# Kernel optimization log

Measured on AMD Instinct MI355X. Metric: run time of the kernel, lower is better.

Reference implementation:

```python
import jax, jax.numpy as jnp
import numpy as np

B, S, D, H = 2, 2048, 1024, 16
DK = D // H  # 64
THETA = 10000.0


def setup_inputs() -> dict:
    key = jax.random.key(0)
    ks = jax.random.split(key, 5)
    scale = 1.0 / np.sqrt(D)
    return {
        "x": jax.random.normal(ks[0], (B, S, D), dtype=jnp.float32),
        "Wq": jax.random.normal(ks[1], (D, D), dtype=jnp.float32) * scale,
        "Wk": jax.random.normal(ks[2], (D, D), dtype=jnp.float32) * scale,
        "Wv": jax.random.normal(ks[3], (D, D), dtype=jnp.float32) * scale,
        "Wo": jax.random.normal(ks[4], (D, D), dtype=jnp.float32) * scale,
    }


def _rope(t):
    # t: (B, H, S, DK); interleaved-pair rotary embedding with positions 0..S-1
    s = t.shape[-2]
    inv_freq = 1.0 / (THETA ** (jnp.arange(0, DK, 2, dtype=jnp.float32) / DK))  # (DK/2,)
    ang = jnp.arange(s, dtype=jnp.float32)[:, None] * inv_freq[None, :]  # (S, DK/2)
    cos, sin = jnp.cos(ang), jnp.sin(ang)
    x1 = t[..., 0::2]
    x2 = t[..., 1::2]
    r1 = x1 * cos - x2 * sin
    r2 = x1 * sin + x2 * cos
    return jnp.stack([r1, r2], axis=-1).reshape(t.shape)


def reference(x, Wq, Wk, Wv, Wo):
    # Projections (Linear: y = x @ W^T), split heads -> (B, H, S, DK)
    def proj(W):
        y = jnp.einsum('bsd,ed->bse', x, W)
        return y.reshape(B, S, H, DK).transpose(0, 2, 1, 3)

    Q = _rope(proj(Wq))
    K = _rope(proj(Wk))
    V = proj(Wv)

    scores = jnp.einsum('bhqd,bhkd->bhqk', Q, K)
    scores = jnp.clip(scores, -80.0, 80.0)
    causal = jnp.tril(jnp.ones((S, S), dtype=bool))  # (S, S)
    scores = jnp.where(causal, scores, -jnp.inf)
    weights = jax.nn.softmax(scores / np.sqrt(DK), axis=-1)
    att = jnp.einsum('bhqk,bhkd->bhqd', weights, V)
    att = att.transpose(0, 2, 1, 3).reshape(B, S, D)
    return jnp.einsum('bsd,ed->bse', att, Wo)
```

## Files before the change

kernel.cpp:

```cpp
#include <hip/hip_runtime.h>
#include <hip/hip_bf16.h>

#define B_  2
#define S_  2048
#define D_  1024
#define H_  16
#define DK_ 64
#define BH_ (B_*H_)
#define M_  (B_*S_)

typedef __attribute__((ext_vector_type(8))) short bf16x8;
typedef __attribute__((ext_vector_type(4))) float f32x4;

__device__ inline float bf2f(unsigned short u) {
    return __uint_as_float(((unsigned)u) << 16);
}
__device__ inline unsigned short f2bf(float f) {
    unsigned u = __float_as_uint(f);
    u += 0x7fffu + ((u >> 16) & 1u);
    return (unsigned short)(u >> 16);
}
__device__ inline unsigned short f2bf_hw(float f) {
    __hip_bfloat16 h = __float2bfloat16(f);
    return *reinterpret_cast<unsigned short*>(&h);
}
__device__ inline unsigned packbf2(float lo, float hi) {
    return (unsigned)f2bf_hw(lo) | ((unsigned)f2bf_hw(hi) << 16);
}

__device__ inline void gld16(const void* g, void* l) {
    __builtin_amdgcn_global_load_lds(
        (const __attribute__((address_space(1))) unsigned int*)g,
        (__attribute__((address_space(3))) unsigned int*)l, 16, 0, 0);
}

__global__ void cast_f32_to_bf16(const float* __restrict__ src,
                                 unsigned short* __restrict__ dst, int n) {
    int i = (blockIdx.x * blockDim.x + threadIdx.x) * 4;
    int stride = gridDim.x * blockDim.x * 4;
    for (int j = i; j < n; j += stride) {
        float4 v = *reinterpret_cast<const float4*>(src + j);
        ushort4 o;
        o.x = f2bf(v.x); o.y = f2bf(v.y); o.z = f2bf(v.z); o.w = f2bf(v.w);
        *reinterpret_cast<ushort4*>(dst + j) = o;
    }
}

__global__ void cast4_f32_to_bf16(const float* __restrict__ s0, const float* __restrict__ s1,
                                  const float* __restrict__ s2, const float* __restrict__ s3,
                                  unsigned short* __restrict__ d0, unsigned short* __restrict__ d1,
                                  unsigned short* __restrict__ d2, unsigned short* __restrict__ d3) {
    const float* s; unsigned short* d;
    switch (blockIdx.y) {
        case 0: s = s0; d = d0; break;
        case 1: s = s1; d = d1; break;
        case 2: s = s2; d = d2; break;
        default: s = s3; d = d3; break;
    }
    int j = (blockIdx.x * blockDim.x + threadIdx.x) * 4;
    float4 v = *reinterpret_cast<const float4*>(s + j);
    ushort4 o;
    o.x = f2bf(v.x); o.y = f2bf(v.y); o.z = f2bf(v.z); o.w = f2bf(v.w);
    *reinterpret_cast<ushort4*>(d + j) = o;
}

#define BMQ 128
#define BNQ 128

__global__ __launch_bounds__(256)
void gemm_qkv(const unsigned short* __restrict__ A, const unsigned short* __restrict__ Wcat,
              unsigned short* __restrict__ Qf, unsigned short* __restrict__ Kf,
              unsigned short* __restrict__ Vf) {
    __shared__ unsigned short As[BMQ * 64];
    __shared__ unsigned short Bs[BNQ * 64];
    const int K = D_;
    const int tid  = threadIdx.x;
    const int lane = tid & 63;
    const int wid  = tid >> 6;
    const int wm = wid & 1, wn = wid >> 1;
    const int m0 = blockIdx.y * BMQ, n0 = blockIdx.x * BNQ;
    const int g  = lane >> 4, cl = lane & 15;

    f32x4 acc[4][4];
#pragma unroll
    for (int i = 0; i < 4; i++)
#pragma unroll
        for (int j = 0; j < 4; j++) acc[i][j] = f32x4{0.f, 0.f, 0.f, 0.f};

    const int srow = tid >> 3;
    const unsigned short* Asrc[4];
    const unsigned short* Bsrc[4];
#pragma unroll
    for (int q = 0; q < 4; q++) {
        int row = srow + q * 32;
        Asrc[q] = A    + (long)(m0 + row) * K + (((tid & 7) ^ (srow & 7)) * 8);
        Bsrc[q] = Wcat + (long)(n0 + row) * K + (((tid & 7) ^ (srow & 7)) * 8);
    }

    for (int k0 = 0; k0 < K; k0 += 64) {
        __syncthreads();
#pragma unroll
        for (int q = 0; q < 4; q++) gld16(Asrc[q] + k0, As + tid * 8 + q * 2048);
#pragma unroll
        for (int q = 0; q < 4; q++) gld16(Bsrc[q] + k0, Bs + tid * 8 + q * 2048);
        __syncthreads();

#pragma unroll
        for (int kk = 0; kk < 2; kk++) {
            bf16x8 af[4], bfr[4];
#pragma unroll
            for (int i = 0; i < 4; i++) {
                int row = wm*64 + i*16 + cl;
                af[i]  = *reinterpret_cast<const bf16x8*>(As + row * 64 + (((kk*4 + g) ^ (cl & 7)) * 8));
            }
#pragma unroll
            for (int j = 0; j < 4; j++) {
                int row = wn*64 + j*16 + cl;
                bfr[j] = *reinterpret_cast<const bf16x8*>(Bs + row * 64 + (((kk*4 + g) ^ (cl & 7)) * 8));
            }
#pragma unroll
            for (int i = 0; i < 4; i++)
#pragma unroll
                for (int j = 0; j < 4; j++)
                    acc[i][j] = __builtin_amdgcn_mfma_f32_16x16x32_bf16(af[i], bfr[j], acc[i][j], 0, 0, 0);
        }
    }

    const int mat = n0 >> 10;
    if (mat < 2) {
        float invf[4];
#pragma unroll
        for (int jj = 0; jj < 4; jj++)
            invf[jj] = exp2f(-(float)(jj*8 + (cl >> 1)) * 0.4152410118569779f);
#pragma unroll
        for (int i = 0; i < 4; i++) {
#pragma unroll
            for (int jj = 0; jj < 4; jj++) {
                const int gcl = (n0 & 1023) + wn*64 + jj*16 + cl;
                const int hh = gcl >> 6;
                const int dk = jj*16 + cl;
#pragma unroll
                for (int rr = 0; rr < 4; rr++) {
                    int gr = m0 + wm*64 + i*16 + g*4 + rr;
                    int bb = gr >> 11, s = gr & (S_ - 1);
                    float v = acc[i][jj][rr];
                    float p = __shfl_xor(v, 1);
                    float ang = (float)s * invf[jj];
                    float sn = __sinf(ang), cs = __cosf(ang);
                    float r = (cl & 1) ? fmaf(v, cs, p * sn) : fmaf(v, cs, -p * sn);
                    long idx;
                    if (mat == 0) {
                        const int lane_p = (s & 15) | (((dk >> 3) & 3) << 4);
                        idx = ((long)(bb*H_ + hh) * 128 + (s >> 4)) * 1024
                            + (dk >> 5) * 512 + lane_p * 8 + (dk & 7);
                        Qf[idx] = f2bf_hw(r);
                    } else {
                        const int vv = s & 63;
                        const int ng = ((vv >> 5) << 1) | ((vv >> 2) & 1);
                        const int slot = ((vv & 31) >> 3) * 4 + (vv & 3);
                        const int lane_p = slot | (((dk >> 3) & 3) << 4);
                        idx = (((long)(bb*H_ + hh) * 32 + (s >> 6)) * 4 + ng) * 1024
                            + (dk >> 5) * 512 + lane_p * 8 + (dk & 7);
                        Kf[idx] = f2bf_hw(r);
                    }
                }
            }
        }
    } else {
#pragma unroll
        for (int i = 0; i < 4; i++) {
#pragma unroll
            for (int jj = 0; jj < 4; jj++) {
                const int gcl = (n0 & 1023) + wn*64 + jj*16 + cl;
                const int hh = gcl >> 6;
                const int sbase = m0 + wm*64 + i*16 + g*4;
                const int bb = sbase >> 11, s0l = sbase & (S_ - 1);
                const int lane_p = cl | (((s0l >> 3) & 3) << 4);
                const int e0 = s0l & 7;
                ushort4 o;
                o.x = f2bf_hw(acc[i][jj][0]); o.y = f2bf_hw(acc[i][jj][1]);
                o.z = f2bf_hw(acc[i][jj][2]); o.w = f2bf_hw(acc[i][jj][3]);
                long idx = ((long)(bb*H_ + hh) * 4 + jj) * 32768
                         + (long)(s0l >> 5) * 512 + lane_p * 8 + e0;
                *reinterpret_cast<ushort4*>(Vf + idx) = o;
            }
        }
    }
}

#define BM 64
#define BN 128

__global__ __launch_bounds__(256)
void gemm_out(const unsigned short* __restrict__ A, const unsigned short* __restrict__ Bw,
              float* __restrict__ Cf) {
    __shared__ unsigned short As[BM * 64];
    __shared__ unsigned short Bs[BN * 64];
    const int K = D_;
    const int tid  = threadIdx.x;
    const int lane = tid & 63;
    const int wid  = tid >> 6;
    const int wm = wid & 1, wn = wid >> 1;
    const int m0 = blockIdx.y * BM, n0 = blockIdx.x * BN;
    const int g  = lane >> 4, cl = lane & 15;

    f32x4 acc[2][4];
#pragma unroll
    for (int i = 0; i < 2; i++)
#pragma unroll
        for (int j = 0; j < 4; j++) acc[i][j] = f32x4{0.f, 0.f, 0.f, 0.f};

    const int srow = tid >> 3;
    const unsigned short* Asrc[2];
    const unsigned short* Bsrc[4];
#pragma unroll
    for (int q = 0; q < 2; q++) {
        int row = srow + q * 32;
        Asrc[q] = A + (long)(m0 + row) * K + (((tid & 7) ^ (srow & 7)) * 8);
    }
#pragma unroll
    for (int q = 0; q < 4; q++) {
        int row = srow + q * 32;
        Bsrc[q] = Bw + (long)(n0 + row) * K + (((tid & 7) ^ (srow & 7)) * 8);
    }

    for (int k0 = 0; k0 < K; k0 += 64) {
        __syncthreads();
#pragma unroll
        for (int q = 0; q < 2; q++) gld16(Asrc[q] + k0, As + tid * 8 + q * 2048);
#pragma unroll
        for (int q = 0; q < 4; q++) gld16(Bsrc[q] + k0, Bs + tid * 8 + q * 2048);
        __syncthreads();

#pragma unroll
        for (int kk = 0; kk < 2; kk++) {
            bf16x8 af[2], bfr[4];
#pragma unroll
            for (int i = 0; i < 2; i++) {
                int row = wm*32 + i*16 + cl;
                af[i]  = *reinterpret_cast<const bf16x8*>(As + row * 64 + (((kk*4 + g) ^ (cl & 7)) * 8));
            }
#pragma unroll
            for (int j = 0; j < 4; j++) {
                int row = wn*64 + j*16 + cl;
                bfr[j] = *reinterpret_cast<const bf16x8*>(Bs + row * 64 + (((kk*4 + g) ^ (cl & 7)) * 8));
            }
#pragma unroll
            for (int i = 0; i < 2; i++)
#pragma unroll
                for (int j = 0; j < 4; j++)
                    acc[i][j] = __builtin_amdgcn_mfma_f32_16x16x32_bf16(af[i], bfr[j], acc[i][j], 0, 0, 0);
        }
    }

#pragma unroll
    for (int i = 0; i < 2; i++)
#pragma unroll
        for (int j = 0; j < 4; j++)
#pragma unroll
            for (int rr = 0; rr < 4; rr++) {
                int gr = m0 + wm*32 + i*16 + g*4 + rr;
                int gc = n0 + wn*64 + j*16 + cl;
                Cf[(long)gr * D_ + gc] = acc[i][j][rr];
            }
}

#define WQ    32
#define KVBLK 64

__global__ __launch_bounds__(256)
void flash_attn(const unsigned short* __restrict__ Qf, const unsigned short* __restrict__ Kf,
                const unsigned short* __restrict__ Vf, unsigned short* __restrict__ Att) {
    __shared__ __align__(16) char smem[17408];
    const int tid  = threadIdx.x;
    const int lane = tid & 63;
    const int wid  = tid >> 6;
    const int g = lane >> 4, cl = lane & 15;
    const int bh = blockIdx.x & (BH_ - 1);
    const int pr = blockIdx.x >> 5;
    const int b = bh >> 4, h = bh & (H_ - 1);

    f32x4* Ol = reinterpret_cast<f32x4*>(smem);
    float* Ll = reinterpret_cast<float*>(smem + 16384);

    const unsigned short* Qb = Qf + (long)bh * 131072;
    const unsigned short* Kb = Kf + (long)bh * 131072;
    const unsigned short* Vb = Vf + (long)bh * 131072;

    const float RS = 0.125f * 1.44269504f;
    const float RB = -10.f * 1.44269504f;

    for (int half = 0; half < 2; half++) {
        const int qt = half ? (S_/WQ - 1 - pr) : pr;
        const int q0 = qt * WQ;
        const int nt = (q0 + WQ + KVBLK - 1) / KVBLK;

        bf16x8 aq[2][2];
#pragma unroll
        for (int m = 0; m < 2; m++)
#pragma unroll
            for (int c = 0; c < 2; c++)
                aq[m][c] = *reinterpret_cast<const bf16x8*>(Qb + ((q0 >> 4) + m) * 1024 + c * 512 + lane * 8);

        f32x4 o[2][4];
#pragma unroll
        for (int m = 0; m < 2; m++)
#pragma unroll
            for (int t = 0; t < 4; t++) o[m][t] = f32x4{0.f, 0.f, 0.f, 0.f};
        float lp[2] = {0.f, 0.f};

        for (int j = wid; j < nt; j += 4) {
            const int kv0 = j * KVBLK;
            bf16x8 bk[4][2];
#pragma unroll
            for (int n = 0; n < 4; n++)
#pragma unroll
                for (int c = 0; c < 2; c++)
                    bk[n][c] = *reinterpret_cast<const bf16x8*>(Kb + (j * 4 + n) * 1024 + c * 512 + lane * 8);
            f32x4 sc[2][4];
#pragma unroll
            for (int m = 0; m < 2; m++)
#pragma unroll
                for (int n = 0; n < 4; n++) {
                    f32x4 z = f32x4{0.f, 0.f, 0.f, 0.f};
                    z = __builtin_amdgcn_mfma_f32_16x16x32_bf16(bk[n][0], aq[m][0], z, 0, 0, 0);
                    z = __builtin_amdgcn_mfma_f32_16x16x32_bf16(bk[n][1], aq[m][1], z, 0, 0, 0);
                    sc[m][n] = z;
                }

            bf16x8 bv[4][2];
#pragma unroll
            for (int t = 0; t < 4; t++)
#pragma unroll
                for (int c = 0; c < 2; c++)
                    bv[t][c] = *reinterpret_cast<const bf16x8*>(Vb + (long)t * 32768 + ((kv0 >> 5) + c) * 512 + lane * 8);

            const bool diag = (kv0 + KVBLK - 1 > q0);
#pragma unroll
            for (int m = 0; m < 2; m++) {
                const int q = q0 + m*16 + cl;
                union { unsigned u[4]; bf16x8 v; } w0, w1;
#pragma unroll
                for (int n = 0; n < 4; n++) {
                    float p4[4];
#pragma unroll
                    for (int rr = 0; rr < 4; rr++) {
                        float u2 = fminf(fmaf(sc[m][n][rr], RS, RB), 0.f);
                        float pe = __builtin_amdgcn_exp2f(u2);
                        if (diag) {
                            const int kv = kv0 + ((n >> 1) << 5) + (g << 3) + ((n & 1) << 2) + rr;
                            if (kv > q) pe = 0.f;
                        }
                        p4[rr] = pe;
                    }
                    lp[m] += (p4[0] + p4[1]) + (p4[2] + p4[3]);
                    const unsigned lo = packbf2(p4[0], p4[1]);
                    const unsigned hi = packbf2(p4[2], p4[3]);
                    if (n == 0)      { w0.u[0] = lo; w0.u[1] = hi; }
                    else if (n == 1) { w0.u[2] = lo; w0.u[3] = hi; }
                    else if (n == 2) { w1.u[0] = lo; w1.u[1] = hi; }
                    else             { w1.u[2] = lo; w1.u[3] = hi; }
                }
#pragma unroll
                for (int t = 0; t < 4; t++) {
                    o[m][t] = __builtin_amdgcn_mfma_f32_16x16x32_bf16(w0.v, bv[t][0], o[m][t], 0, 0, 0);
                    o[m][t] = __builtin_amdgcn_mfma_f32_16x16x32_bf16(w1.v, bv[t][1], o[m][t], 0, 0, 0);
                }
            }
        }

        __syncthreads();
        if (wid == 1 || wid == 3) {
            const int slot = wid >> 1;
#pragma unroll
            for (int m = 0; m < 2; m++) {
#pragma unroll
                for (int t = 0; t < 4; t++)
                    Ol[(slot*8 + m*4 + t)*64 + lane] = o[m][t];
                Ll[(slot*2 + m)*64 + lane] = lp[m];
            }
        }
        __syncthreads();
        if (wid == 0 || wid == 2) {
            const int slot = wid >> 1;
#pragma unroll
            for (int m = 0; m < 2; m++) {
#pragma unroll
                for (int t = 0; t < 4; t++) {
                    f32x4 v = Ol[(slot*8 + m*4 + t)*64 + lane];
#pragma unroll
                    for (int rr = 0; rr < 4; rr++) o[m][t][rr] += v[rr];
                }
                lp[m] += Ll[(slot*2 + m)*64 + lane];
            }
        }
        __syncthreads();
        if (wid == 2) {
#pragma unroll
            for (int m = 0; m < 2; m++) {
#pragma unroll
                for (int t = 0; t < 4; t++)
                    Ol[(m*4 + t)*64 + lane] = o[m][t];
                Ll[m*64 + lane] = lp[m];
            }
        }
        __syncthreads();
        if (wid == 0) {
#pragma unroll
            for (int m = 0; m < 2; m++) {
#pragma unroll
                for (int t = 0; t < 4; t++) {
                    f32x4 v = Ol[(m*4 + t)*64 + lane];
#pragma unroll
                    for (int rr = 0; rr < 4; rr++) o[m][t][rr] += v[rr];
                }
                lp[m] += Ll[m*64 + lane];
                lp[m] += __shfl_xor(lp[m], 16);
                lp[m] += __shfl_xor(lp[m], 32);
            }
            float linv[2][4];
#pragma unroll
            for (int m = 0; m < 2; m++)
#pragma unroll
                for (int rr = 0; rr < 4; rr++)
                    linv[m][rr] = 1.0f / __shfl(lp[m], g*4 + rr);
#pragma unroll
            for (int m = 0; m < 2; m++)
#pragma unroll
                for (int t = 0; t < 4; t++)
#pragma unroll
                    for (int rr = 0; rr < 4; rr++) {
                        const int q = q0 + m*16 + g*4 + rr;
                        const int d = t*16 + cl;
                        Att[(long)(b * S_ + q) * D_ + h * DK_ + d] = f2bf_hw(o[m][t][rr] * linv[m][rr]);
                    }
        }
        __syncthreads();
    }
}

extern "C" void kernel_launch(void* const* d_in, const int* in_sizes, int n_in,
                              void* d_out, int out_size, void* d_ws, size_t ws_size,
                              hipStream_t stream) {
    const float* x  = (const float*)d_in[0];
    const float* Wq = (const float*)d_in[1];
    const float* Wk = (const float*)d_in[2];
    const float* Wv = (const float*)d_in[3];
    const float* Wo = (const float*)d_in[4];
    float* out = (float*)d_out;

    char* ws = (char*)d_ws;
    unsigned short* xb  = (unsigned short*)(ws);
    unsigned short* att = xb;
    unsigned short* WqB = (unsigned short*)(ws + (8  << 20));
    unsigned short* WkB = (unsigned short*)(ws + (10 << 20));
    unsigned short* WvB = (unsigned short*)(ws + (12 << 20));
    unsigned short* WoB = (unsigned short*)(ws + (14 << 20));
    unsigned short* Qf  = (unsigned short*)(ws + (16 << 20));
    unsigned short* Kf  = (unsigned short*)(ws + (24 << 20));
    unsigned short* Vf  = (unsigned short*)(ws + (32 << 20));

    const int nx = B_ * S_ * D_;
    cast_f32_to_bf16<<<4096, 256, 0, stream>>>(x, xb, nx);
    cast4_f32_to_bf16<<<dim3(1024, 4), 256, 0, stream>>>(Wq, Wk, Wv, Wo, WqB, WkB, WvB, WoB);

    dim3 qkvgrid(3 * D_ / BNQ, M_ / BMQ);
    gemm_qkv<<<qkvgrid, 256, 0, stream>>>(xb, WqB, Qf, Kf, Vf);

    flash_attn<<<(S_/WQ/2) * BH_, 256, 0, stream>>>(Qf, Kf, Vf, att);

    dim3 ogrid(D_ / BN, M_ / BM);
    gemm_out<<<ogrid, 256, 0, stream>>>(att, WoB, out);
}
```

Measured before the change: 117.2 us.

## Restructure attention work split, merge cast kernels, and precompute RoPE table

```diff
diff --git a/kernel.cpp b/kernel.cpp
--- a/kernel.cpp
+++ b/kernel.cpp
@@ -34,30 +34,30 @@
         (__attribute__((address_space(3))) unsigned int*)l, 16, 0, 0);
 }
 
-__global__ void cast_f32_to_bf16(const float* __restrict__ src,
-                                 unsigned short* __restrict__ dst, int n) {
-    int i = (blockIdx.x * blockDim.x + threadIdx.x) * 4;
-    int stride = gridDim.x * blockDim.x * 4;
-    for (int j = i; j < n; j += stride) {
-        float4 v = *reinterpret_cast<const float4*>(src + j);
-        ushort4 o;
-        o.x = f2bf(v.x); o.y = f2bf(v.y); o.z = f2bf(v.z); o.w = f2bf(v.w);
-        *reinterpret_cast<ushort4*>(dst + j) = o;
-    }
-}
-
-__global__ void cast4_f32_to_bf16(const float* __restrict__ s0, const float* __restrict__ s1,
-                                  const float* __restrict__ s2, const float* __restrict__ s3,
-                                  unsigned short* __restrict__ d0, unsigned short* __restrict__ d1,
-                                  unsigned short* __restrict__ d2, unsigned short* __restrict__ d3) {
-    const float* s; unsigned short* d;
+__global__ void rope_tab(float2* __restrict__ Tab) {
+    int idx = blockIdx.x * blockDim.x + threadIdx.x;
+    int s = idx >> 5, i = idx & 31;
+    float ang = (float)s * exp2f(-(float)i * 0.4152410118569779f);
+    float sn, cs;
+    sincosf(ang, &sn, &cs);
+    Tab[idx] = float2{cs, sn};
+}
+
+__global__ void cast_all(const float* __restrict__ x,
+                         const float* __restrict__ w0, const float* __restrict__ w1,
+                         const float* __restrict__ w2, const float* __restrict__ w3,
+                         unsigned short* __restrict__ xb,
+                         unsigned short* __restrict__ d0, unsigned short* __restrict__ d1,
+                         unsigned short* __restrict__ d2, unsigned short* __restrict__ d3) {
+    const float* s; unsigned short* d; long base;
     switch (blockIdx.y) {
-        case 0: s = s0; d = d0; break;
-        case 1: s = s1; d = d1; break;
-        case 2: s = s2; d = d2; break;
-        default: s = s3; d = d3; break;
-    }
-    int j = (blockIdx.x * blockDim.x + threadIdx.x) * 4;
+        case 0: s = w0; d = d0; base = 0; break;
+        case 1: s = w1; d = d1; base = 0; break;
+        case 2: s = w2; d = d2; base = 0; break;
+        case 3: s = w3; d = d3; base = 0; break;
+        default: s = x; d = xb; base = (long)(blockIdx.y - 4) << 20; break;
+    }
+    long j = base + (blockIdx.x * blockDim.x + threadIdx.x) * 4;
     float4 v = *reinterpret_cast<const float4*>(s + j);
     ushort4 o;
     o.x = f2bf(v.x); o.y = f2bf(v.y); o.z = f2bf(v.z); o.w = f2bf(v.w);
@@ -69,6 +69,7 @@
 
 __global__ __launch_bounds__(256)
 void gemm_qkv(const unsigned short* __restrict__ A, const unsigned short* __restrict__ Wcat,
+              const float2* __restrict__ Tab,
               unsigned short* __restrict__ Qf, unsigned short* __restrict__ Kf,
               unsigned short* __restrict__ Vf) {
     __shared__ unsigned short As[BMQ * 64];
@@ -128,10 +129,6 @@
 
     const int mat = n0 >> 10;
     if (mat < 2) {
-        float invf[4];
-#pragma unroll
-        for (int jj = 0; jj < 4; jj++)
-            invf[jj] = exp2f(-(float)(jj*8 + (cl >> 1)) * 0.4152410118569779f);
 #pragma unroll
         for (int i = 0; i < 4; i++) {
 #pragma unroll
@@ -139,15 +136,15 @@
                 const int gcl = (n0 & 1023) + wn*64 + jj*16 + cl;
                 const int hh = gcl >> 6;
                 const int dk = jj*16 + cl;
+                const int ifr = jj*8 + (cl >> 1);
 #pragma unroll
                 for (int rr = 0; rr < 4; rr++) {
                     int gr = m0 + wm*64 + i*16 + g*4 + rr;
                     int bb = gr >> 11, s = gr & (S_ - 1);
                     float v = acc[i][jj][rr];
                     float p = __shfl_xor(v, 1);
-                    float ang = (float)s * invf[jj];
-                    float sn = __sinf(ang), cs = __cosf(ang);
-                    float r = (cl & 1) ? fmaf(v, cs, p * sn) : fmaf(v, cs, -p * sn);
+                    float2 t = Tab[s * 32 + ifr];
+                    float r = (cl & 1) ? fmaf(v, t.x, p * t.y) : fmaf(v, t.x, -p * t.y);
                     long idx;
                     if (mat == 0) {
                         const int lane_p = (s & 15) | (((dk >> 3) & 3) << 4);
@@ -265,23 +262,20 @@
             }
 }
 
-#define WQ    32
 #define KVBLK 64
 
 __global__ __launch_bounds__(256)
 void flash_attn(const unsigned short* __restrict__ Qf, const unsigned short* __restrict__ Kf,
                 const unsigned short* __restrict__ Vf, unsigned short* __restrict__ Att) {
-    __shared__ __align__(16) char smem[17408];
     const int tid  = threadIdx.x;
     const int lane = tid & 63;
     const int wid  = tid >> 6;
     const int g = lane >> 4, cl = lane & 15;
     const int bh = blockIdx.x & (BH_ - 1);
-    const int pr = blockIdx.x >> 5;
+    const int qb = (S_/128 - 1) - (int)(blockIdx.x >> 5);
     const int b = bh >> 4, h = bh & (H_ - 1);
-
-    f32x4* Ol = reinterpret_cast<f32x4*>(smem);
-    float* Ll = reinterpret_cast<float*>(smem + 16384);
+    const int q0 = qb * 128 + wid * 32;
+    const int nt = (q0 + 32 + 63) >> 6;
 
     const unsigned short* Qb = Qf + (long)bh * 131072;
     const unsigned short* Kb = Kf + (long)bh * 131072;
@@ -290,153 +284,101 @@
     const float RS = 0.125f * 1.44269504f;
     const float RB = -10.f * 1.44269504f;
 
-    for (int half = 0; half < 2; half++) {
-        const int qt = half ? (S_/WQ - 1 - pr) : pr;
-        const int q0 = qt * WQ;
-        const int nt = (q0 + WQ + KVBLK - 1) / KVBLK;
-
-        bf16x8 aq[2][2];
+    bf16x8 aq[2][2];
+#pragma unroll
+    for (int m = 0; m < 2; m++)
+#pragma unroll
+        for (int c = 0; c < 2; c++)
+            aq[m][c] = *reinterpret_cast<const bf16x8*>(Qb + ((q0 >> 4) + m) * 1024 + c * 512 + lane * 8);
+
+    f32x4 o[2][4];
+#pragma unroll
+    for (int m = 0; m < 2; m++)
+#pragma unroll
+        for (int t = 0; t < 4; t++) o[m][t] = f32x4{0.f, 0.f, 0.f, 0.f};
+    float lp[2] = {0.f, 0.f};
+
+    for (int j = 0; j < nt; j++) {
+        const int kv0 = j * KVBLK;
+        bf16x8 bk[4][2];
+#pragma unroll
+        for (int n = 0; n < 4; n++)
+#pragma unroll
+            for (int c = 0; c < 2; c++)
+                bk[n][c] = *reinterpret_cast<const bf16x8*>(Kb + (j * 4 + n) * 1024 + c * 512 + lane * 8);
+        f32x4 sc[2][4];
 #pragma unroll
         for (int m = 0; m < 2; m++)
 #pragma unroll
+            for (int n = 0; n < 4; n++) {
+                f32x4 z = f32x4{0.f, 0.f, 0.f, 0.f};
+                z = __builtin_amdgcn_mfma_f32_16x16x32_bf16(bk[n][0], aq[m][0], z, 0, 0, 0);
+                z = __builtin_amdgcn_mfma_f32_16x16x32_bf16(bk[n][1], aq[m][1], z, 0, 0, 0);
+                sc[m][n] = z;
+            }
+
+        bf16x8 bv[4][2];
+#pragma unroll
+        for (int t = 0; t < 4; t++)
+#pragma unroll
             for (int c = 0; c < 2; c++)
-                aq[m][c] = *reinterpret_cast<const bf16x8*>(Qb + ((q0 >> 4) + m) * 1024 + c * 512 + lane * 8);
-
-        f32x4 o[2][4];
-#pragma unroll
-        for (int m = 0; m < 2; m++)
-#pragma unroll
-            for (int t = 0; t < 4; t++) o[m][t] = f32x4{0.f, 0.f, 0.f, 0.f};
-        float lp[2] = {0.f, 0.f};
-
-        for (int j = wid; j < nt; j += 4) {
-            const int kv0 = j * KVBLK;
-            bf16x8 bk[4][2];
-#pragma unroll
-            for (int n = 0; n < 4; n++)
-#pragma unroll
-                for (int c = 0; c < 2; c++)
-                    bk[n][c] = *reinterpret_cast<const bf16x8*>(Kb + (j * 4 + n) * 1024 + c * 512 + lane * 8);
-            f32x4 sc[2][4];
-#pragma unroll
-            for (int m = 0; m < 2; m++)
-#pragma unroll
-                for (int n = 0; n < 4; n++) {
-                    f32x4 z = f32x4{0.f, 0.f, 0.f, 0.f};
-                    z = __builtin_amdgcn_mfma_f32_16x16x32_bf16(bk[n][0], aq[m][0], z, 0, 0, 0);
-                    z = __builtin_amdgcn_mfma_f32_16x16x32_bf16(bk[n][1], aq[m][1], z, 0, 0, 0);
-                    sc[m][n] = z;
+                bv[t][c] = *reinterpret_cast<const bf16x8*>(Vb + (long)t * 32768 + ((kv0 >> 5) + c) * 512 + lane * 8);
+
+        const bool diag = (kv0 + KVBLK - 1 > q0);
+#pragma unroll
+        for (int m = 0; m < 2; m++) {
+            const int q = q0 + m*16 + cl;
+            union { unsigned u[4]; bf16x8 v; } w0, w1;
+#pragma unroll
+            for (int n = 0; n < 4; n++) {
+                float p4[4];
+#pragma unroll
+                for (int rr = 0; rr < 4; rr++) {
+                    float u2 = fminf(fmaf(sc[m][n][rr], RS, RB), 0.f);
+                    float pe = __builtin_amdgcn_exp2f(u2);
+                    if (diag) {
+                        const int kv = kv0 + ((n >> 1) << 5) + (g << 3) + ((n & 1) << 2) + rr;
+                        if (kv > q) pe = 0.f;
+                    }
+                    p4[rr] = pe;
                 }
-
-            bf16x8 bv[4][2];
-#pragma unroll
-            for (int t = 0; t < 4; t++)
-#pragma unroll
-                for (int c = 0; c < 2; c++)
-                    bv[t][c] = *reinterpret_cast<const bf16x8*>(Vb + (long)t * 32768 + ((kv0 >> 5) + c) * 512 + lane * 8);
-
-            const bool diag = (kv0 + KVBLK - 1 > q0);
-#pragma unroll
-            for (int m = 0; m < 2; m++) {
-                const int q = q0 + m*16 + cl;
-                union { unsigned u[4]; bf16x8 v; } w0, w1;
-#pragma unroll
-                for (int n = 0; n < 4; n++) {
-                    float p4[4];
-#pragma unroll
-                    for (int rr = 0; rr < 4; rr++) {
-                        float u2 = fminf(fmaf(sc[m][n][rr], RS, RB), 0.f);
-                        float pe = __builtin_amdgcn_exp2f(u2);
-                        if (diag) {
-                            const int kv = kv0 + ((n >> 1) << 5) + (g << 3) + ((n & 1) << 2) + rr;
-                            if (kv > q) pe = 0.f;
-                        }
-                        p4[rr] = pe;
-                    }
-                    lp[m] += (p4[0] + p4[1]) + (p4[2] + p4[3]);
-                    const unsigned lo = packbf2(p4[0], p4[1]);
-                    const unsigned hi = packbf2(p4[2], p4[3]);
-                    if (n == 0)      { w0.u[0] = lo; w0.u[1] = hi; }
-                    else if (n == 1) { w0.u[2] = lo; w0.u[3] = hi; }
-                    else if (n == 2) { w1.u[0] = lo; w1.u[1] = hi; }
-                    else             { w1.u[2] = lo; w1.u[3] = hi; }
-                }
-#pragma unroll
-                for (int t = 0; t < 4; t++) {
-                    o[m][t] = __builtin_amdgcn_mfma_f32_16x16x32_bf16(w0.v, bv[t][0], o[m][t], 0, 0, 0);
-                    o[m][t] = __builtin_amdgcn_mfma_f32_16x16x32_bf16(w1.v, bv[t][1], o[m][t], 0, 0, 0);
-                }
+                lp[m] += (p4[0] + p4[1]) + (p4[2] + p4[3]);
+                const unsigned lo = packbf2(p4[0], p4[1]);
+                const unsigned hi = packbf2(p4[2], p4[3]);
+                if (n == 0)      { w0.u[0] = lo; w0.u[1] = hi; }
+                else if (n == 1) { w0.u[2] = lo; w0.u[3] = hi; }
+                else if (n == 2) { w1.u[0] = lo; w1.u[1] = hi; }
+                else             { w1.u[2] = lo; w1.u[3] = hi; }
+            }
+#pragma unroll
+            for (int t = 0; t < 4; t++) {
+                o[m][t] = __builtin_amdgcn_mfma_f32_16x16x32_bf16(w0.v, bv[t][0], o[m][t], 0, 0, 0);
+                o[m][t] = __builtin_amdgcn_mfma_f32_16x16x32_bf16(w1.v, bv[t][1], o[m][t], 0, 0, 0);
             }
         }
-
-        __syncthreads();
-        if (wid == 1 || wid == 3) {
-            const int slot = wid >> 1;
-#pragma unroll
-            for (int m = 0; m < 2; m++) {
-#pragma unroll
-                for (int t = 0; t < 4; t++)
-                    Ol[(slot*8 + m*4 + t)*64 + lane] = o[m][t];
-                Ll[(slot*2 + m)*64 + lane] = lp[m];
-            }
-        }
-        __syncthreads();
-        if (wid == 0 || wid == 2) {
-            const int slot = wid >> 1;
-#pragma unroll
-            for (int m = 0; m < 2; m++) {
-#pragma unroll
-                for (int t = 0; t < 4; t++) {
-                    f32x4 v = Ol[(slot*8 + m*4 + t)*64 + lane];
-#pragma unroll
-                    for (int rr = 0; rr < 4; rr++) o[m][t][rr] += v[rr];
-                }
-                lp[m] += Ll[(slot*2 + m)*64 + lane];
-            }
-        }
-        __syncthreads();
-        if (wid == 2) {
-#pragma unroll
-            for (int m = 0; m < 2; m++) {
-#pragma unroll
-                for (int t = 0; t < 4; t++)
-                    Ol[(m*4 + t)*64 + lane] = o[m][t];
-                Ll[m*64 + lane] = lp[m];
-            }
-        }
-        __syncthreads();
-        if (wid == 0) {
-#pragma unroll
-            for (int m = 0; m < 2; m++) {
-#pragma unroll
-                for (int t = 0; t < 4; t++) {
-                    f32x4 v = Ol[(m*4 + t)*64 + lane];
-#pragma unroll
-                    for (int rr = 0; rr < 4; rr++) o[m][t][rr] += v[rr];
-                }
-                lp[m] += Ll[m*64 + lane];
-                lp[m] += __shfl_xor(lp[m], 16);
-                lp[m] += __shfl_xor(lp[m], 32);
-            }
-            float linv[2][4];
-#pragma unroll
-            for (int m = 0; m < 2; m++)
-#pragma unroll
-                for (int rr = 0; rr < 4; rr++)
-                    linv[m][rr] = 1.0f / __shfl(lp[m], g*4 + rr);
-#pragma unroll
-            for (int m = 0; m < 2; m++)
-#pragma unroll
-                for (int t = 0; t < 4; t++)
-#pragma unroll
-                    for (int rr = 0; rr < 4; rr++) {
-                        const int q = q0 + m*16 + g*4 + rr;
-                        const int d = t*16 + cl;
-                        Att[(long)(b * S_ + q) * D_ + h * DK_ + d] = f2bf_hw(o[m][t][rr] * linv[m][rr]);
-                    }
-        }
-        __syncthreads();
-    }
+    }
+
+#pragma unroll
+    for (int m = 0; m < 2; m++) {
+        lp[m] += __shfl_xor(lp[m], 16);
+        lp[m] += __shfl_xor(lp[m], 32);
+    }
+    float linv[2][4];
+#pragma unroll
+    for (int m = 0; m < 2; m++)
+#pragma unroll
+        for (int rr = 0; rr < 4; rr++)
+            linv[m][rr] = 1.0f / __shfl(lp[m], g*4 + rr);
+#pragma unroll
+    for (int m = 0; m < 2; m++)
+#pragma unroll
+        for (int t = 0; t < 4; t++)
+#pragma unroll
+            for (int rr = 0; rr < 4; rr++) {
+                const int q = q0 + m*16 + g*4 + rr;
+                const int d = t*16 + cl;
+                Att[(long)(b * S_ + q) * D_ + h * DK_ + d] = f2bf_hw(o[m][t][rr] * linv[m][rr]);
+            }
 }
 
 extern "C" void kernel_launch(void* const* d_in, const int* in_sizes, int n_in,
@@ -460,14 +402,15 @@
     unsigned short* Kf  = (unsigned short*)(ws + (24 << 20));
     unsigned short* Vf  = (unsigned short*)(ws + (32 << 20));
 
-    const int nx = B_ * S_ * D_;
-    cast_f32_to_bf16<<<4096, 256, 0, stream>>>(x, xb, nx);
-    cast4_f32_to_bf16<<<dim3(1024, 4), 256, 0, stream>>>(Wq, Wk, Wv, Wo, WqB, WkB, WvB, WoB);
+    float2* Tab = (float2*)d_out;
+
+    rope_tab<<<256, 256, 0, stream>>>(Tab);
+    cast_all<<<dim3(1024, 8), 256, 0, stream>>>(x, Wq, Wk, Wv, Wo, xb, WqB, WkB, WvB, WoB);
 
     dim3 qkvgrid(3 * D_ / BNQ, M_ / BMQ);
-    gemm_qkv<<<qkvgrid, 256, 0, stream>>>(xb, WqB, Qf, Kf, Vf);
-
-    flash_attn<<<(S_/WQ/2) * BH_, 256, 0, stream>>>(Qf, Kf, Vf, att);
+    gemm_qkv<<<qkvgrid, 256, 0, stream>>>(xb, WqB, Tab, Qf, Kf, Vf);
+
+    flash_attn<<<(S_/128) * BH_, 256, 0, stream>>>(Qf, Kf, Vf, att);
 
     dim3 ogrid(D_ / BN, M_ / BM);
     gemm_out<<<ogrid, 256, 0, stream>>>(att, WoB, out);
```

Result: slower. 152.6 us (+30.2%).

## Triple-buffer QKV GEMM with 512 threads; compute softmax row sums via MFMA

Applied to the files above, without the earlier changes.

```diff
diff --git a/kernel.cpp b/kernel.cpp
--- a/kernel.cpp
+++ b/kernel.cpp
@@ -12,9 +12,6 @@
 typedef __attribute__((ext_vector_type(8))) short bf16x8;
 typedef __attribute__((ext_vector_type(4))) float f32x4;
 
-__device__ inline float bf2f(unsigned short u) {
-    return __uint_as_float(((unsigned)u) << 16);
-}
 __device__ inline unsigned short f2bf(float f) {
     unsigned u = __float_as_uint(f);
     u += 0x7fffu + ((u >> 16) & 1u);
@@ -67,63 +64,89 @@
 #define BMQ 128
 #define BNQ 128
 
-__global__ __launch_bounds__(256)
+__global__ __launch_bounds__(512)
 void gemm_qkv(const unsigned short* __restrict__ A, const unsigned short* __restrict__ Wcat,
               unsigned short* __restrict__ Qf, unsigned short* __restrict__ Kf,
               unsigned short* __restrict__ Vf) {
-    __shared__ unsigned short As[BMQ * 64];
-    __shared__ unsigned short Bs[BNQ * 64];
-    const int K = D_;
+    __shared__ unsigned short As[3][8192];
+    __shared__ unsigned short Bs[3][8192];
     const int tid  = threadIdx.x;
     const int lane = tid & 63;
     const int wid  = tid >> 6;
-    const int wm = wid & 1, wn = wid >> 1;
+    const int wm = wid & 3;
+    const int wn = wid >> 2;
     const int m0 = blockIdx.y * BMQ, n0 = blockIdx.x * BNQ;
     const int g  = lane >> 4, cl = lane & 15;
 
-    f32x4 acc[4][4];
-#pragma unroll
-    for (int i = 0; i < 4; i++)
+    f32x4 acc[2][4];
+#pragma unroll
+    for (int i = 0; i < 2; i++)
 #pragma unroll
         for (int j = 0; j < 4; j++) acc[i][j] = f32x4{0.f, 0.f, 0.f, 0.f};
 
-    const int srow = tid >> 3;
-    const unsigned short* Asrc[4];
-    const unsigned short* Bsrc[4];
-#pragma unroll
-    for (int q = 0; q < 4; q++) {
-        int row = srow + q * 32;
-        Asrc[q] = A    + (long)(m0 + row) * K + (((tid & 7) ^ (srow & 7)) * 8);
-        Bsrc[q] = Wcat + (long)(n0 + row) * K + (((tid & 7) ^ (srow & 7)) * 8);
-    }
-
-    for (int k0 = 0; k0 < K; k0 += 64) {
-        __syncthreads();
-#pragma unroll
-        for (int q = 0; q < 4; q++) gld16(Asrc[q] + k0, As + tid * 8 + q * 2048);
-#pragma unroll
-        for (int q = 0; q < 4; q++) gld16(Bsrc[q] + k0, Bs + tid * 8 + q * 2048);
-        __syncthreads();
-
+    const int srow = tid >> 2;
+    const unsigned short* Asrc[2];
+    const unsigned short* Bsrc[2];
+#pragma unroll
+    for (int q = 0; q < 2; q++) {
+        const int c = (((tid & 3) << 1) | q) ^ (srow & 7);
+        Asrc[q] = A    + (long)(m0 + srow) * D_ + c * 8;
+        Bsrc[q] = Wcat + (long)(n0 + srow) * D_ + c * 8;
+    }
+
+    auto STAGE = [&](int t) {
+        unsigned short* Ab = &As[t % 3][0];
+        unsigned short* Bb = &Bs[t % 3][0];
+        const int k0 = t * 64;
+#pragma unroll
+        for (int q = 0; q < 2; q++) {
+            gld16(Asrc[q] + k0, Ab + q * 4096 + tid * 8);
+            gld16(Bsrc[q] + k0, Bb + q * 4096 + tid * 8);
+        }
+    };
+
+    auto COMPUTE = [&](int bufi) {
+        const unsigned short* Ab = &As[bufi][0];
+        const unsigned short* Bb = &Bs[bufi][0];
+        bf16x8 bfr[4][2];
+#pragma unroll
+        for (int j = 0; j < 4; j++)
+#pragma unroll
+            for (int kk = 0; kk < 2; kk++) {
+                const int r = wn * 64 + j * 16 + cl;
+                const int p = (kk * 4 + g) ^ (r & 7);
+                bfr[j][kk] = *reinterpret_cast<const bf16x8*>(Bb + (p & 1) * 4096 + r * 32 + (p >> 1) * 8);
+            }
 #pragma unroll
         for (int kk = 0; kk < 2; kk++) {
-            bf16x8 af[4], bfr[4];
-#pragma unroll
-            for (int i = 0; i < 4; i++) {
-                int row = wm*64 + i*16 + cl;
-                af[i]  = *reinterpret_cast<const bf16x8*>(As + row * 64 + (((kk*4 + g) ^ (cl & 7)) * 8));
-            }
-#pragma unroll
-            for (int j = 0; j < 4; j++) {
-                int row = wn*64 + j*16 + cl;
-                bfr[j] = *reinterpret_cast<const bf16x8*>(Bs + row * 64 + (((kk*4 + g) ^ (cl & 7)) * 8));
-            }
-#pragma unroll
-            for (int i = 0; i < 4; i++)
+            bf16x8 af[2];
+#pragma unroll
+            for (int i = 0; i < 2; i++) {
+                const int r = wm * 32 + i * 16 + cl;
+                const int p = (kk * 4 + g) ^ (r & 7);
+                af[i] = *reinterpret_cast<const bf16x8*>(Ab + (p & 1) * 4096 + r * 32 + (p >> 1) * 8);
+            }
+#pragma unroll
+            for (int i = 0; i < 2; i++)
 #pragma unroll
                 for (int j = 0; j < 4; j++)
-                    acc[i][j] = __builtin_amdgcn_mfma_f32_16x16x32_bf16(af[i], bfr[j], acc[i][j], 0, 0, 0);
-        }
+                    acc[i][j] = __builtin_amdgcn_mfma_f32_16x16x32_bf16(af[i], bfr[j][kk], acc[i][j], 0, 0, 0);
+        }
+    };
+
+    STAGE(0); STAGE(1); STAGE(2);
+
+#pragma unroll 1
+    for (int t = 0; t < 16; ++t) {
+        if (t <= 13)      asm volatile("s_waitcnt vmcnt(8)" ::: "memory");
+        else if (t == 14) asm volatile("s_waitcnt vmcnt(4)" ::: "memory");
+        else              asm volatile("s_waitcnt vmcnt(0)" ::: "memory");
+        __builtin_amdgcn_s_barrier();
+        asm volatile("" ::: "memory");
+        COMPUTE(t % 3);
+        asm volatile("" ::: "memory");
+        __builtin_amdgcn_s_barrier();
+        if (t < 13) STAGE(t + 3);
     }
 
     const int mat = n0 >> 10;
@@ -133,7 +156,7 @@
         for (int jj = 0; jj < 4; jj++)
             invf[jj] = exp2f(-(float)(jj*8 + (cl >> 1)) * 0.4152410118569779f);
 #pragma unroll
-        for (int i = 0; i < 4; i++) {
+        for (int i = 0; i < 2; i++) {
 #pragma unroll
             for (int jj = 0; jj < 4; jj++) {
                 const int gcl = (n0 & 1023) + wn*64 + jj*16 + cl;
@@ -141,7 +164,7 @@
                 const int dk = jj*16 + cl;
 #pragma unroll
                 for (int rr = 0; rr < 4; rr++) {
-                    int gr = m0 + wm*64 + i*16 + g*4 + rr;
+                    int gr = m0 + wm*32 + i*16 + g*4 + rr;
                     int bb = gr >> 11, s = gr & (S_ - 1);
                     float v = acc[i][jj][rr];
                     float p = __shfl_xor(v, 1);
@@ -168,12 +191,12 @@
         }
     } else {
 #pragma unroll
-        for (int i = 0; i < 4; i++) {
+        for (int i = 0; i < 2; i++) {
 #pragma unroll
             for (int jj = 0; jj < 4; jj++) {
                 const int gcl = (n0 & 1023) + wn*64 + jj*16 + cl;
                 const int hh = gcl >> 6;
-                const int sbase = m0 + wm*64 + i*16 + g*4;
+                const int sbase = m0 + wm*32 + i*16 + g*4;
                 const int bb = sbase >> 11, s0l = sbase & (S_ - 1);
                 const int lane_p = cl | (((s0l >> 3) & 3) << 4);
                 const int e0 = s0l & 7;
@@ -271,7 +294,7 @@
 __global__ __launch_bounds__(256)
 void flash_attn(const unsigned short* __restrict__ Qf, const unsigned short* __restrict__ Kf,
                 const unsigned short* __restrict__ Vf, unsigned short* __restrict__ Att) {
-    __shared__ __align__(16) char smem[17408];
+    __shared__ __align__(16) char smem[20480];
     const int tid  = threadIdx.x;
     const int lane = tid & 63;
     const int wid  = tid >> 6;
@@ -281,7 +304,6 @@
     const int b = bh >> 4, h = bh & (H_ - 1);
 
     f32x4* Ol = reinterpret_cast<f32x4*>(smem);
-    float* Ll = reinterpret_cast<float*>(smem + 16384);
 
     const unsigned short* Qb = Qf + (long)bh * 131072;
     const unsigned short* Kb = Kf + (long)bh * 131072;
@@ -289,6 +311,10 @@
 
     const float RS = 0.125f * 1.44269504f;
     const float RB = -10.f * 1.44269504f;
+
+    bf16x8 onesv;
+#pragma unroll
+    for (int e = 0; e < 8; e++) onesv[e] = (short)0x3F80;
 
     for (int half = 0; half < 2; half++) {
         const int qt = half ? (S_/WQ - 1 - pr) : pr;
@@ -302,12 +328,13 @@
             for (int c = 0; c < 2; c++)
                 aq[m][c] = *reinterpret_cast<const bf16x8*>(Qb + ((q0 >> 4) + m) * 1024 + c * 512 + lane * 8);
 
-        f32x4 o[2][4];
-#pragma unroll
-        for (int m = 0; m < 2; m++)
+        f32x4 o[2][4], ol[2];
+#pragma unroll
+        for (int m = 0; m < 2; m++) {
 #pragma unroll
             for (int t = 0; t < 4; t++) o[m][t] = f32x4{0.f, 0.f, 0.f, 0.f};
-        float lp[2] = {0.f, 0.f};
+            ol[m] = f32x4{0.f, 0.f, 0.f, 0.f};
+        }
 
         for (int j = wid; j < nt; j += 4) {
             const int kv0 = j * KVBLK;
@@ -345,15 +372,13 @@
                     float p4[4];
 #pragma unroll
                     for (int rr = 0; rr < 4; rr++) {
-                        float u2 = fminf(fmaf(sc[m][n][rr], RS, RB), 0.f);
-                        float pe = __builtin_amdgcn_exp2f(u2);
+                        float pe = __builtin_amdgcn_exp2f(fmaf(sc[m][n][rr], RS, RB));
                         if (diag) {
                             const int kv = kv0 + ((n >> 1) << 5) + (g << 3) + ((n & 1) << 2) + rr;
                             if (kv > q) pe = 0.f;
                         }
                         p4[rr] = pe;
                     }
-                    lp[m] += (p4[0] + p4[1]) + (p4[2] + p4[3]);
                     const unsigned lo = packbf2(p4[0], p4[1]);
                     const unsigned hi = packbf2(p4[2], p4[3]);
                     if (n == 0)      { w0.u[0] = lo; w0.u[1] = hi; }
@@ -366,6 +391,8 @@
                     o[m][t] = __builtin_amdgcn_mfma_f32_16x16x32_bf16(w0.v, bv[t][0], o[m][t], 0, 0, 0);
                     o[m][t] = __builtin_amdgcn_mfma_f32_16x16x32_bf16(w1.v, bv[t][1], o[m][t], 0, 0, 0);
                 }
+                ol[m] = __builtin_amdgcn_mfma_f32_16x16x32_bf16(w0.v, onesv, ol[m], 0, 0, 0);
+                ol[m] = __builtin_amdgcn_mfma_f32_16x16x32_bf16(w1.v, onesv, ol[m], 0, 0, 0);
             }
         }
 
@@ -376,8 +403,8 @@
             for (int m = 0; m < 2; m++) {
 #pragma unroll
                 for (int t = 0; t < 4; t++)
-                    Ol[(slot*8 + m*4 + t)*64 + lane] = o[m][t];
-                Ll[(slot*2 + m)*64 + lane] = lp[m];
+                    Ol[((slot*2 + m)*5 + t)*64 + lane] = o[m][t];
+                Ol[((slot*2 + m)*5 + 4)*64 + lane] = ol[m];
             }
         }
         __syncthreads();
@@ -387,11 +414,13 @@
             for (int m = 0; m < 2; m++) {
 #pragma unroll
                 for (int t = 0; t < 4; t++) {
-                    f32x4 v = Ol[(slot*8 + m*4 + t)*64 + lane];
+                    f32x4 v = Ol[((slot*2 + m)*5 + t)*64 + lane];
 #pragma unroll
                     for (int rr = 0; rr < 4; rr++) o[m][t][rr] += v[rr];
                 }
-                lp[m] += Ll[(slot*2 + m)*64 + lane];
+                f32x4 vl = Ol[((slot*2 + m)*5 + 4)*64 + lane];
+#pragma unroll
+                for (int rr = 0; rr < 4; rr++) ol[m][rr] += vl[rr];
             }
         }
         __syncthreads();
@@ -400,8 +429,8 @@
             for (int m = 0; m < 2; m++) {
 #pragma unroll
                 for (int t = 0; t < 4; t++)
-                    Ol[(m*4 + t)*64 + lane] = o[m][t];
-                Ll[m*64 + lane] = lp[m];
+                    Ol[(m*5 + t)*64 + lane] = o[m][t];
+                Ol[(m*5 + 4)*64 + lane] = ol[m];
             }
         }
         __syncthreads();
@@ -410,30 +439,28 @@
             for (int m = 0; m < 2; m++) {
 #pragma unroll
                 for (int t = 0; t < 4; t++) {
-                    f32x4 v = Ol[(m*4 + t)*64 + lane];
+                    f32x4 v = Ol[(m*5 + t)*64 + lane];
 #pragma unroll
                     for (int rr = 0; rr < 4; rr++) o[m][t][rr] += v[rr];
                 }
-                lp[m] += Ll[m*64 + lane];
-                lp[m] += __shfl_xor(lp[m], 16);
-                lp[m] += __shfl_xor(lp[m], 32);
-            }
-            float linv[2][4];
-#pragma unroll
-            for (int m = 0; m < 2; m++)
-#pragma unroll
-                for (int rr = 0; rr < 4; rr++)
-                    linv[m][rr] = 1.0f / __shfl(lp[m], g*4 + rr);
-#pragma unroll
-            for (int m = 0; m < 2; m++)
+                f32x4 vl = Ol[(m*5 + 4)*64 + lane];
+#pragma unroll
+                for (int rr = 0; rr < 4; rr++) ol[m][rr] += vl[rr];
+            }
+#pragma unroll
+            for (int m = 0; m < 2; m++) {
+                float linv[4];
+#pragma unroll
+                for (int rr = 0; rr < 4; rr++) linv[rr] = 1.0f / ol[m][rr];
 #pragma unroll
                 for (int t = 0; t < 4; t++)
 #pragma unroll
                     for (int rr = 0; rr < 4; rr++) {
                         const int q = q0 + m*16 + g*4 + rr;
                         const int d = t*16 + cl;
-                        Att[(long)(b * S_ + q) * D_ + h * DK_ + d] = f2bf_hw(o[m][t][rr] * linv[m][rr]);
+                        Att[(long)(b * S_ + q) * D_ + h * DK_ + d] = f2bf_hw(o[m][t][rr] * linv[rr]);
                     }
+            }
         }
         __syncthreads();
     }
@@ -465,7 +492,7 @@
     cast4_f32_to_bf16<<<dim3(1024, 4), 256, 0, stream>>>(Wq, Wk, Wv, Wo, WqB, WkB, WvB, WoB);
 
     dim3 qkvgrid(3 * D_ / BNQ, M_ / BMQ);
-    gemm_qkv<<<qkvgrid, 256, 0, stream>>>(xb, WqB, Qf, Kf, Vf);
+    gemm_qkv<<<qkvgrid, 512, 0, stream>>>(xb, WqB, Qf, Kf, Vf);
 
     flash_attn<<<(S_/WQ/2) * BH_, 256, 0, stream>>>(Qf, Kf, Vf, att);
 
```

Result: slower. 128.1 us (+9.4%).
